# Optimization experiments

Hardware: AMD Instinct MI355X
Metric: run time of the kernel (lower is better)

Reference implementation:

```python
import jax, jax.numpy as jnp
import numpy as np

B, S, H = 4, 2048, 1024
E, F = 8, 4096
K = 2  # hardcoded top-k in the original forward


def setup_inputs() -> dict:
    key = jax.random.key(0)
    ks = jax.random.split(key, 8)
    scale = 0.02
    x = jax.random.normal(ks[0], (B, S, H), dtype=jnp.float32)
    Wr = jax.random.normal(ks[1], (H, E), dtype=jnp.float32) * scale
    br = jnp.zeros((E,), dtype=jnp.float32)
    W1 = jax.random.normal(ks[2], (E, H, F), dtype=jnp.float32) * scale
    b1 = jnp.zeros((E, F), dtype=jnp.float32)
    W2 = jax.random.normal(ks[3], (E, F, H), dtype=jnp.float32) * scale
    b2 = jnp.zeros((E, H), dtype=jnp.float32)
    return {"x": x, "Wr": Wr, "br": br, "W1": W1, "b1": b1, "W2": W2, "b2": b2}


def reference(x, Wr, br, W1, b1, W2, b2):
    # Router: [B,S,H] @ [H,E] -> [B,S,E]
    router_logits = jnp.einsum('bsh,he->bse', x, Wr) + br
    router_probs = jax.nn.softmax(router_logits, axis=-1)
    top_k_probs, top_k_indices = jax.lax.top_k(router_probs, K)
    top_k_probs = top_k_probs / jnp.sum(top_k_probs, axis=-1, keepdims=True)
    # NOTE: original code weights EVERY selected expert by the normalized top-1 prob.
    p0 = top_k_probs[..., 0]  # [B,S]

    combined = jnp.zeros((B, S, H), dtype=x.dtype)
    for e in range(E):
        mask = jnp.any(top_k_indices == e, axis=-1)  # [B,S]
        # Dense FFN (dropout deterministic => identity); gelu approximate (flax default)
        h = jax.nn.gelu(jnp.einsum('bsh,hf->bsf', x, W1[e]) + b1[e])
        y = jnp.einsum('bsf,fh->bsh', h, W2[e]) + b2[e]
        combined = combined + jnp.where(mask[..., None], y * p0[..., None], 0.0)
    return combined
```

## Files before the change

kernel.cpp:

```cpp
#include <hip/hip_runtime.h>
#include <hip/hip_bf16.h>


typedef __bf16 bf16;
typedef __attribute__((ext_vector_type(4))) __bf16 bf16x4;
typedef __attribute__((ext_vector_type(8))) __bf16 bf16x8;
typedef __attribute__((ext_vector_type(4))) float f32x4;

#define GLD16(g, l) __builtin_amdgcn_global_load_lds( \
    (__attribute__((address_space(1))) void*)(g),      \
    (__attribute__((address_space(3))) void*)(l), 16, 0, 0)

__device__ __forceinline__ float gelu_fast(float v) {
  float u = v * fmaf(v * v, 0.0713548162726f, 1.5957691216057308f);
  return v * __builtin_amdgcn_rcpf(1.0f + __expf(-u));
}

__global__ __launch_bounds__(256) void router_kernel(
    const float* __restrict__ x, const float* __restrict__ Wr,
    const float* __restrict__ br, int* __restrict__ e01,
    float* __restrict__ p0arr) {
  int wv = threadIdx.x >> 6;
  int l = threadIdx.x & 63;
  int t = blockIdx.x * 4 + wv;
  float acc[8];
#pragma unroll
  for (int e = 0; e < 8; e++) acc[e] = 0.f;
  const float* xr = x + (size_t)t * 1024;
#pragma unroll
  for (int i = 0; i < 16; i++) {
    int h = l + i * 64;
    float xv = xr[h];
    const float4* w4 = (const float4*)(Wr + h * 8);
    float4 wa = w4[0], wb = w4[1];
    acc[0] += xv * wa.x; acc[1] += xv * wa.y; acc[2] += xv * wa.z; acc[3] += xv * wa.w;
    acc[4] += xv * wb.x; acc[5] += xv * wb.y; acc[6] += xv * wb.z; acc[7] += xv * wb.w;
  }
#pragma unroll
  for (int e = 0; e < 8; e++) {
    float v = acc[e];
#pragma unroll
    for (int m = 1; m < 64; m <<= 1) v += __shfl_xor(v, m, 64);
    acc[e] = v + br[e];
  }
  int i1 = 0; float m1 = acc[0];
#pragma unroll
  for (int e = 1; e < 8; e++) { if (acc[e] > m1) { m1 = acc[e]; i1 = e; } }
  int i2 = -1; float m2 = -3.4e38f;
#pragma unroll
  for (int e = 0; e < 8; e++) { if (e != i1 && acc[e] > m2) { m2 = acc[e]; i2 = e; } }
  if (l == 0) {
    e01[t] = i1 | (i2 << 8);
    p0arr[t] = 1.0f / (1.0f + __expf(m2 - m1));
  }
}

__global__ __launch_bounds__(1024) void slots_kernel(
    const int* __restrict__ e01, int* __restrict__ meta,
    int* __restrict__ slot1, int* __restrict__ slot2) {
  __shared__ int wtot[16];
  int tid = threadIdx.x;
  int l = tid & 63, wv = tid >> 6;
  int t0 = tid * 8;
  int i1[8], i2[8];
#pragma unroll
  for (int i = 0; i < 8; i++) {
    int ee = e01[t0 + i];
    i1[i] = ee & 255;
    i2[i] = (ee >> 8) & 255;
  }
  int offl[9];
  int running = 0;
  for (int e = 0; e < 8; e++) {
    offl[e] = running;
    int cthread = 0;
#pragma unroll
    for (int i = 0; i < 8; i++) cthread += (i1[i] == e) + (i2[i] == e);
    int inc = cthread;
#pragma unroll
    for (int d = 1; d < 64; d <<= 1) {
      int v = __shfl_up(inc, d, 64);
      if (l >= d) inc += v;
    }
    if (l == 63) wtot[wv] = inc;
    __syncthreads();
    int wbase = 0, total = 0;
#pragma unroll
    for (int w = 0; w < 16; w++) {
      int tw = wtot[w];
      wbase += (w < wv) ? tw : 0;
      total += tw;
    }
    int base = running + wbase + (inc - cthread);
#pragma unroll
    for (int i = 0; i < 8; i++) {
      if (i1[i] == e) { slot1[t0 + i] = base; base++; }
      if (i2[i] == e) { slot2[t0 + i] = base; base++; }
    }
    running += total;
    __syncthreads();
  }
  offl[8] = running;
  if (tid == 0) {
#pragma unroll
    for (int e = 0; e < 9; e++) meta[e] = offl[e];
    int nt = 0;
    for (int e = 0; e < 8; e++)
      for (int r = offl[e]; r < offl[e + 1]; r += 256)
        meta[16 + (nt++)] = r | (e << 20);
    meta[10] = nt;
  }
}

__global__ __launch_bounds__(256) void gather_kernel(
    const float* __restrict__ x, const int* __restrict__ slot1,
    const int* __restrict__ slot2, bf16* __restrict__ Xg) {
  int t = blockIdx.x;
  int s1 = slot1[t], s2 = slot2[t];
  float4 v = ((const float4*)(x + (size_t)t * 1024))[threadIdx.x];
  bf16x4 bv = { (bf16)v.x, (bf16)v.y, (bf16)v.z, (bf16)v.w };
  *(bf16x4*)(Xg + (size_t)s1 * 1024 + threadIdx.x * 4) = bv;
  *(bf16x4*)(Xg + (size_t)s2 * 1024 + threadIdx.x * 4) = bv;
}

__global__ __launch_bounds__(256) void tconv_kernel(
    const float* __restrict__ in, bf16* __restrict__ out, int R, int C) {
  __shared__ float tile[64][65];
  size_t base = (size_t)blockIdx.z * R * C;
  int gr0 = blockIdx.y * 64, gc0 = blockIdx.x * 64;
  int tr = threadIdx.x >> 4;
  int tc4 = (threadIdx.x & 15) * 4;
#pragma unroll
  for (int i = 0; i < 4; i++) {
    int r = tr + i * 16;
    float4 v = *(const float4*)&in[base + (size_t)(gr0 + r) * C + gc0 + tc4];
    tile[r][tc4] = v.x; tile[r][tc4 + 1] = v.y;
    tile[r][tc4 + 2] = v.z; tile[r][tc4 + 3] = v.w;
  }
  __syncthreads();
  int rr0 = (threadIdx.x & 7) * 8;
  int cc0 = threadIdx.x >> 3;
#pragma unroll
  for (int i = 0; i < 2; i++) {
    int cc = cc0 + i * 32;
    bf16x8 v;
#pragma unroll
    for (int k = 0; k < 8; k++) v[k] = (bf16)tile[rr0 + k][cc];
    *(bf16x8*)&out[base + (size_t)(gc0 + cc) * R + gr0 + rr0] = v;
  }
}

__device__ __forceinline__ bool xcd_tile(int b, int ntiles, int nshift,
                                         int& m_idx, int& n_tile) {
  int xcd = b & 7, j = b >> 3;
  int total = ntiles << nshift;
  int q = total >> 3, r = total & 7;
  int cnt = q + (xcd < r ? 1 : 0);
  if (j >= cnt) return false;
  int start = (xcd < r) ? xcd * (q + 1) : r * (q + 1) + (xcd - r) * q;
  int tidx = start + j;
  m_idx = tidx >> nshift;
  n_tile = tidx & ((1 << nshift) - 1);
  return true;
}

__device__ __forceinline__ void gemm256_core(
    const bf16* __restrict__ Abase, const bf16* __restrict__ Bbase,
    int K, int NT, char* smem, f32x4 acc[8][4], int wr, int wc, int l) {
  int tid = threadIdx.x;
  size_t K2 = (size_t)K * 2;
  const char* src[4];
  int dst[4];
#pragma unroll
  for (int i = 0; i < 4; i++) {
    int s = (i & 1) ? (tid + 512) : tid;
    int byteoff = s * 16;
    int p = byteoff >> 7;
    int W = byteoff & 127;
    int L = W ^ ((p & 7) << 4);
    int r = 2 * p + (L >> 6);
    int c = L & 63;
    const char* base = (const char*)((i >= 2) ? Bbase : Abase);
    src[i] = base + (size_t)r * K2 + c;
    dst[i] = ((i >= 2) ? 16384 : 0) + byteoff;
  }
  int offA[8], offB[4];
  int kc16 = (l >> 4) << 4;
#pragma unroll
  for (int mf = 0; mf < 8; mf++) {
    int r = wr * 128 + mf * 16 + (l & 15);
    int p = r >> 1;
    offA[mf] = (p << 7) + ((((r & 1) << 6) | kc16) ^ ((p & 7) << 4));
  }
#pragma unroll
  for (int nf = 0; nf < 4; nf++) {
    int r = wc * 64 + nf * 16 + (l & 15);
    int p = r >> 1;
    offB[nf] = 16384 + (p << 7) + ((((r & 1) << 6) | kc16) ^ ((p & 7) << 4));
  }
#pragma unroll
  for (int t = 0; t < 3; t++) {
    char* bu = smem + t * 32768;
#pragma unroll
    for (int i = 0; i < 4; i++) GLD16(src[i] + t * 64, bu + dst[i]);
  }
  asm volatile("s_waitcnt vmcnt(8)" ::: "memory");
  __builtin_amdgcn_s_barrier();
  for (int t = 0; t < NT; t++) {
    char* bc = smem + (t & 3) * 32768;
    char* bs = smem + ((t + 3) & 3) * 32768;
    bool st = (t + 3) < NT;
    bf16x8 bfr[4], af[4];
#pragma unroll
    for (int nf = 0; nf < 4; nf++) bfr[nf] = *(const bf16x8*)(bc + offB[nf]);
#pragma unroll
    for (int mf = 0; mf < 4; mf++) af[mf] = *(const bf16x8*)(bc + offA[mf]);
    if (st) {
      GLD16(src[0] + (t + 3) * 64, bs + dst[0]);
      GLD16(src[1] + (t + 3) * 64, bs + dst[1]);
    }
    __builtin_amdgcn_s_barrier();
    asm volatile("s_waitcnt lgkmcnt(0)" ::: "memory");
    __builtin_amdgcn_s_setprio(1);
#pragma unroll
    for (int mf = 0; mf < 4; mf++)
#pragma unroll
      for (int nf = 0; nf < 4; nf++)
        acc[mf][nf] = __builtin_amdgcn_mfma_f32_16x16x32_bf16(bfr[nf], af[mf], acc[mf][nf], 0, 0, 0);
    __builtin_amdgcn_s_setprio(0);
    __builtin_amdgcn_s_barrier();
#pragma unroll
    for (int mf = 0; mf < 4; mf++) af[mf] = *(const bf16x8*)(bc + offA[mf + 4]);
    if (st) {
      GLD16(src[2] + (t + 3) * 64, bs + dst[2]);
      GLD16(src[3] + (t + 3) * 64, bs + dst[3]);
    }
    __builtin_amdgcn_s_barrier();
    asm volatile("s_waitcnt lgkmcnt(0)" ::: "memory");
    __builtin_amdgcn_s_setprio(1);
#pragma unroll
    for (int mf = 0; mf < 4; mf++)
#pragma unroll
      for (int nf = 0; nf < 4; nf++)
        acc[mf + 4][nf] = __builtin_amdgcn_mfma_f32_16x16x32_bf16(bfr[nf], af[mf], acc[mf + 4][nf], 0, 0, 0);
    __builtin_amdgcn_s_setprio(0);
    if ((t + 3) < NT)      { asm volatile("s_waitcnt vmcnt(8)" ::: "memory"); }
    else if ((t + 2) < NT) { asm volatile("s_waitcnt vmcnt(4)" ::: "memory"); }
    else if ((t + 1) < NT) { asm volatile("s_waitcnt vmcnt(0)" ::: "memory"); }
    __builtin_amdgcn_s_barrier();
  }
}

__global__ __launch_bounds__(512, 2) void gemm1_kernel(
    const bf16* __restrict__ Xg, const bf16* __restrict__ W1t,
    const float* __restrict__ b1, bf16* __restrict__ hbuf,
    const int* __restrict__ meta) {
  __shared__ __align__(16) char smem[131072];
  int m_idx, n_tile;
  if (!xcd_tile(blockIdx.x, meta[10], 4, m_idx, n_tile)) return;
  int ti = meta[16 + m_idx];
  int row0 = ti & 0xFFFFF;
  int e = ti >> 20;
  int rowEnd = meta[1 + e];
  int tid = threadIdx.x;
  int w = tid >> 6, l = tid & 63;
  int wr = w >> 2, wc = w & 3;
  f32x4 acc[8][4];
#pragma unroll
  for (int a = 0; a < 8; a++)
#pragma unroll
    for (int bb = 0; bb < 4; bb++) acc[a][bb] = (f32x4){0.f, 0.f, 0.f, 0.f};
  gemm256_core(Xg + (size_t)row0 * 1024,
               W1t + ((size_t)e * 4096 + n_tile * 256) * 1024,
               1024, 32, smem, acc, wr, wc, l);
  int mrow = l & 15, nq = (l >> 4) * 4;
  int gn0 = n_tile * 256 + wc * 64 + nq;
  f32x4 bv[4];
#pragma unroll
  for (int nf = 0; nf < 4; nf++)
    bv[nf] = *(const f32x4*)(b1 + e * 4096 + gn0 + nf * 16);
#pragma unroll
  for (int mf = 0; mf < 8; mf++) {
    int gm = row0 + wr * 128 + mf * 16 + mrow;
    if (gm < rowEnd) {
      bf16* rp = hbuf + (size_t)gm * 4096 + gn0;
#pragma unroll
      for (int nf = 0; nf < 4; nf++) {
        bf16x4 o;
#pragma unroll
        for (int jj = 0; jj < 4; jj++)
          o[jj] = (bf16)gelu_fast(acc[mf][nf][jj] + bv[nf][jj]);
        *(bf16x4*)(rp + nf * 16) = o;
      }
    }
  }
}

__global__ __launch_bounds__(512, 2) void gemm2_kernel(
    const bf16* __restrict__ hbuf, const bf16* __restrict__ W2t,
    const float* __restrict__ b2, bf16* __restrict__ yb,
    const int* __restrict__ meta) {
  __shared__ __align__(16) char smem[131072];
  int m_idx, n_tile;
  if (!xcd_tile(blockIdx.x, meta[10], 2, m_idx, n_tile)) return;
  int ti = meta[16 + m_idx];
  int row0 = ti & 0xFFFFF;
  int e = ti >> 20;
  int rowEnd = meta[1 + e];
  int tid = threadIdx.x;
  int w = tid >> 6, l = tid & 63;
  int wr = w >> 2, wc = w & 3;
  f32x4 acc[8][4];
#pragma unroll
  for (int a = 0; a < 8; a++)
#pragma unroll
    for (int bb = 0; bb < 4; bb++) acc[a][bb] = (f32x4){0.f, 0.f, 0.f, 0.f};
  gemm256_core(hbuf + (size_t)row0 * 4096,
               W2t + ((size_t)e * 1024 + n_tile * 256) * 4096,
               4096, 128, smem, acc, wr, wc, l);
  int mrow = l & 15, nq = (l >> 4) * 4;
  int gn0 = n_tile * 256 + wc * 64 + nq;
  f32x4 bv[4];
#pragma unroll
  for (int nf = 0; nf < 4; nf++)
    bv[nf] = *(const f32x4*)(b2 + e * 1024 + gn0 + nf * 16);
#pragma unroll
  for (int mf = 0; mf < 8; mf++) {
    int gm = row0 + wr * 128 + mf * 16 + mrow;
    if (gm < rowEnd) {
      bf16* rp = yb + (size_t)gm * 1024 + gn0;
#pragma unroll
      for (int nf = 0; nf < 4; nf++) {
        bf16x4 o;
#pragma unroll
        for (int jj = 0; jj < 4; jj++)
          o[jj] = (bf16)(acc[mf][nf][jj] + bv[nf][jj]);
        *(bf16x4*)(rp + nf * 16) = o;
      }
    }
  }
}

__global__ __launch_bounds__(256) void combine_kernel(
    const bf16* __restrict__ yb, const int* __restrict__ slot1,
    const int* __restrict__ slot2, const float* __restrict__ p0arr,
    float* __restrict__ out) {
  int t = blockIdx.x;
  int s1 = slot1[t], s2 = slot2[t];
  float w0 = p0arr[t];
  bf16x4 a = *(const bf16x4*)(yb + (size_t)s1 * 1024 + threadIdx.x * 4);
  bf16x4 b = *(const bf16x4*)(yb + (size_t)s2 * 1024 + threadIdx.x * 4);
  float4 o;
  o.x = w0 * ((float)a[0] + (float)b[0]);
  o.y = w0 * ((float)a[1] + (float)b[1]);
  o.z = w0 * ((float)a[2] + (float)b[2]);
  o.w = w0 * ((float)a[3] + (float)b[3]);
  *(float4*)(out + (size_t)t * 1024 + threadIdx.x * 4) = o;
}

extern "C" void kernel_launch(void* const* d_in, const int* in_sizes, int n_in,
                              void* d_out, int out_size, void* d_ws, size_t ws_size,
                              hipStream_t stream) {
  const float* x  = (const float*)d_in[0];
  const float* Wr = (const float*)d_in[1];
  const float* br = (const float*)d_in[2];
  const float* W1 = (const float*)d_in[3];
  const float* b1 = (const float*)d_in[4];
  const float* W2 = (const float*)d_in[5];
  const float* b2 = (const float*)d_in[6];
  float* out = (float*)d_out;

  char* ws = (char*)d_ws;
  int*   meta  = (int*)(ws + 0);
  int*   e01   = (int*)(ws + 4096);
  float* p0    = (float*)(ws + 36864);
  int*   slot1 = (int*)(ws + 69632);
  int*   slot2 = (int*)(ws + 102400);
  bf16*  Xg    = (bf16*)(ws + 135168);
  bf16*  W1t   = (bf16*)(ws + 34213888ULL);
  bf16*  W2t   = (bf16*)(ws + 101322752ULL);
  bf16*  hb    = (bf16*)(ws + 168431616ULL);
  bf16*  yb    = Xg;

  tconv_kernel<<<dim3(64, 16, 8), 256, 0, stream>>>(W1, W1t, 1024, 4096);
  tconv_kernel<<<dim3(16, 64, 8), 256, 0, stream>>>(W2, W2t, 4096, 1024);
  router_kernel<<<2048, 256, 0, stream>>>(x, Wr, br, e01, p0);
  slots_kernel<<<1, 1024, 0, stream>>>(e01, meta, slot1, slot2);
  gather_kernel<<<8192, 256, 0, stream>>>(x, slot1, slot2, Xg);
  gemm1_kernel<<<1152, 512, 0, stream>>>(Xg, W1t, b1, hb, meta);
  gemm2_kernel<<<288, 512, 0, stream>>>(hb, W2t, b2, yb, meta);
  combine_kernel<<<8192, 256, 0, stream>>>(yb, slot1, slot2, p0, out);
}
```

Measured before the change: 789.0 us.

## Shrink GEMM tiles to 256x128 with 4 waves, triple-buffer LDS, fuse prep kernels

The grouped expert GEMMs now use 256x128 output tiles computed by 256-thread blocks (4 waves, 2x2) instead of 256x256 tiles with 8 waves. LDS staging drops from four 32KB buffers to three 24KB buffers with prefetch distance 2, and the tile grids double. Weight transposes and the token gather are merged into one prep kernel launch. The aim is better tail and CU balance for the ragged per-expert tiles and fewer launches, at the cost of lower data reuse per tile and a shallower prefetch pipeline.

```diff
diff --git a/kernel.cpp b/kernel.cpp
--- a/kernel.cpp
+++ b/kernel.cpp
@@ -112,22 +112,34 @@
   }
 }
 
-__global__ __launch_bounds__(256) void gather_kernel(
+__global__ __launch_bounds__(256) void prep_kernel(
     const float* __restrict__ x, const int* __restrict__ slot1,
-    const int* __restrict__ slot2, bf16* __restrict__ Xg) {
-  int t = blockIdx.x;
-  int s1 = slot1[t], s2 = slot2[t];
-  float4 v = ((const float4*)(x + (size_t)t * 1024))[threadIdx.x];
-  bf16x4 bv = { (bf16)v.x, (bf16)v.y, (bf16)v.z, (bf16)v.w };
-  *(bf16x4*)(Xg + (size_t)s1 * 1024 + threadIdx.x * 4) = bv;
-  *(bf16x4*)(Xg + (size_t)s2 * 1024 + threadIdx.x * 4) = bv;
-}
-
-__global__ __launch_bounds__(256) void tconv_kernel(
-    const float* __restrict__ in, bf16* __restrict__ out, int R, int C) {
+    const int* __restrict__ slot2, bf16* __restrict__ Xg,
+    const float* __restrict__ W1, bf16* __restrict__ W1t,
+    const float* __restrict__ W2, bf16* __restrict__ W2t) {
   __shared__ float tile[64][65];
-  size_t base = (size_t)blockIdx.z * R * C;
-  int gr0 = blockIdx.y * 64, gc0 = blockIdx.x * 64;
+  int b = blockIdx.x;
+  if (b < 8192) {
+    int t = b;
+    int s1 = slot1[t], s2 = slot2[t];
+    float4 v = ((const float4*)(x + (size_t)t * 1024))[threadIdx.x];
+    bf16x4 bv = { (bf16)v.x, (bf16)v.y, (bf16)v.z, (bf16)v.w };
+    *(bf16x4*)(Xg + (size_t)s1 * 1024 + threadIdx.x * 4) = bv;
+    *(bf16x4*)(Xg + (size_t)s2 * 1024 + threadIdx.x * 4) = bv;
+    return;
+  }
+  const float* in; bf16* outp; int R, C, bx, by, bz;
+  if (b < 16384) {
+    int b2 = b - 8192;
+    in = W1; outp = W1t; R = 1024; C = 4096;
+    bx = b2 & 63; by = (b2 >> 6) & 15; bz = b2 >> 10;
+  } else {
+    int b2 = b - 16384;
+    in = W2; outp = W2t; R = 4096; C = 1024;
+    bx = b2 & 15; by = (b2 >> 4) & 63; bz = b2 >> 10;
+  }
+  size_t base = (size_t)bz * R * C;
+  int gr0 = by * 64, gc0 = bx * 64;
   int tr = threadIdx.x >> 4;
   int tc4 = (threadIdx.x & 15) * 4;
 #pragma unroll
@@ -146,7 +158,7 @@
     bf16x8 v;
 #pragma unroll
     for (int k = 0; k < 8; k++) v[k] = (bf16)tile[rr0 + k][cc];
-    *(bf16x8*)&out[base + (size_t)(gc0 + cc) * R + gr0 + rr0] = v;
+    *(bf16x8*)&outp[base + (size_t)(gc0 + cc) * R + gr0 + rr0] = v;
   }
 }
 
@@ -164,25 +176,30 @@
   return true;
 }
 
-__device__ __forceinline__ void gemm256_core(
+__device__ __forceinline__ void gemm_core(
     const bf16* __restrict__ Abase, const bf16* __restrict__ Bbase,
     int K, int NT, char* smem, f32x4 acc[8][4], int wr, int wc, int l) {
   int tid = threadIdx.x;
   size_t K2 = (size_t)K * 2;
-  const char* src[4];
-  int dst[4];
+  const char* srcA[4]; const char* srcB[2];
+  int dstA[4], dstB[2];
 #pragma unroll
   for (int i = 0; i < 4; i++) {
-    int s = (i & 1) ? (tid + 512) : tid;
-    int byteoff = s * 16;
-    int p = byteoff >> 7;
-    int W = byteoff & 127;
+    int byteoff = (tid + i * 256) * 16;
+    int p = byteoff >> 7, W = byteoff & 127;
     int L = W ^ ((p & 7) << 4);
-    int r = 2 * p + (L >> 6);
-    int c = L & 63;
-    const char* base = (const char*)((i >= 2) ? Bbase : Abase);
-    src[i] = base + (size_t)r * K2 + c;
-    dst[i] = ((i >= 2) ? 16384 : 0) + byteoff;
+    int r = 2 * p + (L >> 6), c = L & 63;
+    srcA[i] = (const char*)Abase + (size_t)r * K2 + c;
+    dstA[i] = byteoff;
+  }
+#pragma unroll
+  for (int i = 0; i < 2; i++) {
+    int byteoff = (tid + i * 256) * 16;
+    int p = byteoff >> 7, W = byteoff & 127;
+    int L = W ^ ((p & 7) << 4);
+    int r = 2 * p + (L >> 6), c = L & 63;
+    srcB[i] = (const char*)Bbase + (size_t)r * K2 + c;
+    dstB[i] = 16384 + byteoff;
   }
   int offA[8], offB[4];
   int kc16 = (l >> 4) << 4;
@@ -199,25 +216,28 @@
     offB[nf] = 16384 + (p << 7) + ((((r & 1) << 6) | kc16) ^ ((p & 7) << 4));
   }
 #pragma unroll
-  for (int t = 0; t < 3; t++) {
-    char* bu = smem + t * 32768;
-#pragma unroll
-    for (int i = 0; i < 4; i++) GLD16(src[i] + t * 64, bu + dst[i]);
-  }
-  asm volatile("s_waitcnt vmcnt(8)" ::: "memory");
+  for (int t = 0; t < 2; t++) {
+    char* bu = smem + t * 24576;
+#pragma unroll
+    for (int i = 0; i < 4; i++) GLD16(srcA[i] + t * 64, bu + dstA[i]);
+#pragma unroll
+    for (int i = 0; i < 2; i++) GLD16(srcB[i] + t * 64, bu + dstB[i]);
+  }
+  asm volatile("s_waitcnt vmcnt(6)" ::: "memory");
   __builtin_amdgcn_s_barrier();
+  char* bc = smem;
+  char* bs = smem + 2 * 24576;
   for (int t = 0; t < NT; t++) {
-    char* bc = smem + (t & 3) * 32768;
-    char* bs = smem + ((t + 3) & 3) * 32768;
-    bool st = (t + 3) < NT;
+    bool st = (t + 2) < NT;
     bf16x8 bfr[4], af[4];
 #pragma unroll
     for (int nf = 0; nf < 4; nf++) bfr[nf] = *(const bf16x8*)(bc + offB[nf]);
 #pragma unroll
     for (int mf = 0; mf < 4; mf++) af[mf] = *(const bf16x8*)(bc + offA[mf]);
     if (st) {
-      GLD16(src[0] + (t + 3) * 64, bs + dst[0]);
-      GLD16(src[1] + (t + 3) * 64, bs + dst[1]);
+#pragma unroll
+      for (int i = 0; i < 4; i++)
+        GLD16(srcA[i] + (size_t)(t + 2) * 64, bs + dstA[i]);
     }
     __builtin_amdgcn_s_barrier();
     asm volatile("s_waitcnt lgkmcnt(0)" ::: "memory");
@@ -232,8 +252,9 @@
 #pragma unroll
     for (int mf = 0; mf < 4; mf++) af[mf] = *(const bf16x8*)(bc + offA[mf + 4]);
     if (st) {
-      GLD16(src[2] + (t + 3) * 64, bs + dst[2]);
-      GLD16(src[3] + (t + 3) * 64, bs + dst[3]);
+#pragma unroll
+      for (int i = 0; i < 2; i++)
+        GLD16(srcB[i] + (size_t)(t + 2) * 64, bs + dstB[i]);
     }
     __builtin_amdgcn_s_barrier();
     asm volatile("s_waitcnt lgkmcnt(0)" ::: "memory");
@@ -244,37 +265,38 @@
       for (int nf = 0; nf < 4; nf++)
         acc[mf + 4][nf] = __builtin_amdgcn_mfma_f32_16x16x32_bf16(bfr[nf], af[mf], acc[mf + 4][nf], 0, 0, 0);
     __builtin_amdgcn_s_setprio(0);
-    if ((t + 3) < NT)      { asm volatile("s_waitcnt vmcnt(8)" ::: "memory"); }
-    else if ((t + 2) < NT) { asm volatile("s_waitcnt vmcnt(4)" ::: "memory"); }
-    else if ((t + 1) < NT) { asm volatile("s_waitcnt vmcnt(0)" ::: "memory"); }
+    if (st)              { asm volatile("s_waitcnt vmcnt(6)" ::: "memory"); }
+    else if (t + 1 < NT) { asm volatile("s_waitcnt vmcnt(0)" ::: "memory"); }
     __builtin_amdgcn_s_barrier();
-  }
-}
-
-__global__ __launch_bounds__(512, 2) void gemm1_kernel(
+    bc += 24576; if (bc == smem + 73728) bc = smem;
+    bs += 24576; if (bs == smem + 73728) bs = smem;
+  }
+}
+
+__global__ __launch_bounds__(256, 2) void gemm1_kernel(
     const bf16* __restrict__ Xg, const bf16* __restrict__ W1t,
     const float* __restrict__ b1, bf16* __restrict__ hbuf,
     const int* __restrict__ meta) {
-  __shared__ __align__(16) char smem[131072];
+  __shared__ __align__(16) char smem[73728];
   int m_idx, n_tile;
-  if (!xcd_tile(blockIdx.x, meta[10], 4, m_idx, n_tile)) return;
+  if (!xcd_tile(blockIdx.x, meta[10], 5, m_idx, n_tile)) return;
   int ti = meta[16 + m_idx];
   int row0 = ti & 0xFFFFF;
   int e = ti >> 20;
   int rowEnd = meta[1 + e];
   int tid = threadIdx.x;
   int w = tid >> 6, l = tid & 63;
-  int wr = w >> 2, wc = w & 3;
+  int wr = w >> 1, wc = w & 1;
   f32x4 acc[8][4];
 #pragma unroll
   for (int a = 0; a < 8; a++)
 #pragma unroll
     for (int bb = 0; bb < 4; bb++) acc[a][bb] = (f32x4){0.f, 0.f, 0.f, 0.f};
-  gemm256_core(Xg + (size_t)row0 * 1024,
-               W1t + ((size_t)e * 4096 + n_tile * 256) * 1024,
-               1024, 32, smem, acc, wr, wc, l);
+  gemm_core(Xg + (size_t)row0 * 1024,
+            W1t + ((size_t)e * 4096 + n_tile * 128) * 1024,
+            1024, 32, smem, acc, wr, wc, l);
   int mrow = l & 15, nq = (l >> 4) * 4;
-  int gn0 = n_tile * 256 + wc * 64 + nq;
+  int gn0 = n_tile * 128 + wc * 64 + nq;
   f32x4 bv[4];
 #pragma unroll
   for (int nf = 0; nf < 4; nf++)
@@ -296,30 +318,30 @@
   }
 }
 
-__global__ __launch_bounds__(512, 2) void gemm2_kernel(
+__global__ __launch_bounds__(256, 2) void gemm2_kernel(
     const bf16* __restrict__ hbuf, const bf16* __restrict__ W2t,
     const float* __restrict__ b2, bf16* __restrict__ yb,
     const int* __restrict__ meta) {
-  __shared__ __align__(16) char smem[131072];
+  __shared__ __align__(16) char smem[73728];
   int m_idx, n_tile;
-  if (!xcd_tile(blockIdx.x, meta[10], 2, m_idx, n_tile)) return;
+  if (!xcd_tile(blockIdx.x, meta[10], 3, m_idx, n_tile)) return;
   int ti = meta[16 + m_idx];
   int row0 = ti & 0xFFFFF;
   int e = ti >> 20;
   int rowEnd = meta[1 + e];
   int tid = threadIdx.x;
   int w = tid >> 6, l = tid & 63;
-  int wr = w >> 2, wc = w & 3;
+  int wr = w >> 1, wc = w & 1;
   f32x4 acc[8][4];
 #pragma unroll
   for (int a = 0; a < 8; a++)
 #pragma unroll
     for (int bb = 0; bb < 4; bb++) acc[a][bb] = (f32x4){0.f, 0.f, 0.f, 0.f};
-  gemm256_core(hbuf + (size_t)row0 * 4096,
-               W2t + ((size_t)e * 1024 + n_tile * 256) * 4096,
-               4096, 128, smem, acc, wr, wc, l);
+  gemm_core(hbuf + (size_t)row0 * 4096,
+            W2t + ((size_t)e * 1024 + n_tile * 128) * 4096,
+            4096, 128, smem, acc, wr, wc, l);
   int mrow = l & 15, nq = (l >> 4) * 4;
-  int gn0 = n_tile * 256 + wc * 64 + nq;
+  int gn0 = n_tile * 128 + wc * 64 + nq;
   f32x4 bv[4];
 #pragma unroll
   for (int nf = 0; nf < 4; nf++)
@@ -382,12 +404,10 @@
   bf16*  hb    = (bf16*)(ws + 168431616ULL);
   bf16*  yb    = Xg;
 
-  tconv_kernel<<<dim3(64, 16, 8), 256, 0, stream>>>(W1, W1t, 1024, 4096);
-  tconv_kernel<<<dim3(16, 64, 8), 256, 0, stream>>>(W2, W2t, 4096, 1024);
   router_kernel<<<2048, 256, 0, stream>>>(x, Wr, br, e01, p0);
   slots_kernel<<<1, 1024, 0, stream>>>(e01, meta, slot1, slot2);
-  gather_kernel<<<8192, 256, 0, stream>>>(x, slot1, slot2, Xg);
-  gemm1_kernel<<<1152, 512, 0, stream>>>(Xg, W1t, b1, hb, meta);
-  gemm2_kernel<<<288, 512, 0, stream>>>(hb, W2t, b2, yb, meta);
+  prep_kernel<<<24576, 256, 0, stream>>>(x, slot1, slot2, Xg, W1, W1t, W2, W2t);
+  gemm1_kernel<<<2304, 256, 0, stream>>>(Xg, W1t, b1, hb, meta);
+  gemm2_kernel<<<576, 256, 0, stream>>>(hb, W2t, b2, yb, meta);
   combine_kernel<<<8192, 256, 0, stream>>>(yb, slot1, slot2, p0, out);
 }
```

Measured after the change: 734.1 us. -7.0%, faster.
